# Kernel tuning notes

Measured on AMD Instinct MI355X. Metric: run time of the kernel, lower is better.

The kernel has to match this reference:

```python
import jax, jax.numpy as jnp
import numpy as np

NUM_HEADS = 8
ROPE_BASE = 10000.0


def _rope(x):
    # x: [B, S, E]; standard interleaved rotary embedding applied on full embed dim
    B, S, E = x.shape
    half = E // 2
    inv_freq = 1.0 / (ROPE_BASE ** (jnp.arange(0, half, dtype=jnp.float32) * 2.0 / E))
    freqs = jnp.arange(S, dtype=jnp.float32)[:, None] * inv_freq[None, :]  # [S, E/2]
    cos = jnp.cos(freqs)[None]  # [1, S, E/2]
    sin = jnp.sin(freqs)[None]
    x1 = x[..., 0::2]
    x2 = x[..., 1::2]
    r1 = x1 * cos - x2 * sin
    r2 = x1 * sin + x2 * cos
    return jnp.stack([r1, r2], axis=-1).reshape(B, S, E)


def setup_inputs() -> dict:
    key = jax.random.key(0)
    ks = jax.random.split(key, 7)
    B, S, E = 2, 4096, 512
    q = jax.random.normal(ks[0], (B, S, E), dtype=jnp.float32)
    k = jax.random.normal(ks[1], (B, S, E), dtype=jnp.float32)
    v = jax.random.normal(ks[2], (B, S, E), dtype=jnp.float32)
    scale = 1.0 / np.sqrt(E)
    in_proj_w = jax.random.normal(ks[3], (3 * E, E), dtype=jnp.float32) * scale
    in_proj_b = jnp.zeros((3 * E,), dtype=jnp.float32)
    out_proj_w = jax.random.normal(ks[4], (E, E), dtype=jnp.float32) * scale
    out_proj_b = jnp.zeros((E,), dtype=jnp.float32)
    return {"query": q, "key": k, "value": v,
            "in_proj_w": in_proj_w, "in_proj_b": in_proj_b,
            "out_proj_w": out_proj_w, "out_proj_b": out_proj_b}


def reference(query, key, value, in_proj_w, in_proj_b, out_proj_w, out_proj_b):
    B, S, E = query.shape
    H = NUM_HEADS
    D = E // H
    # RoPE applied before projection, as in the original module
    q_in = _rope(query)
    k_in = _rope(key)
    Wq, Wk, Wv = jnp.split(in_proj_w, 3, axis=0)
    bq, bk, bv = jnp.split(in_proj_b, 3, axis=0)
    q = (q_in @ Wq.T + bq).reshape(B, S, H, D).transpose(0, 2, 1, 3)  # [B,H,S,D]
    k = (k_in @ Wk.T + bk).reshape(B, S, H, D).transpose(0, 2, 1, 3)
    v = (value @ Wv.T + bv).reshape(B, S, H, D).transpose(0, 2, 1, 3)
    scores = jnp.einsum('bhqd,bhkd->bhqk', q, k) / jnp.sqrt(jnp.asarray(D, q.dtype))
    weights = jax.nn.softmax(scores, axis=-1)  # [B,H,S,S]
    ctx = jnp.einsum('bhqk,bhkd->bhqd', weights, v)  # [B,H,S,D]
    ctx = ctx.transpose(0, 2, 1, 3).reshape(B, S, E)
    attn_output = ctx @ out_proj_w.T + out_proj_b
    attn_weights = weights.mean(axis=1)  # averaged over heads (need_weights=True default)
    return attn_output, attn_weights
```

## Files before the change

kernel.cpp:

```cpp
#include <hip/hip_runtime.h>
#include <stdint.h>
#include <stddef.h>


#define B_ 2
#define S_ 4096
#define E_ 512
#define H_ 8
#define D_ 64
#define BS_ (B_*S_)

typedef __attribute__((ext_vector_type(8)))  short short8;
typedef __attribute__((ext_vector_type(4)))  float f32x4;
typedef __attribute__((ext_vector_type(16))) float f32x16;
typedef __attribute__((ext_vector_type(4)))  int   i32x4;

#define DEVFN static __device__ __forceinline__

DEVFN short f2bf(float x) {
    unsigned u = __builtin_bit_cast(unsigned, x);
    u += 0x7fffu + ((u >> 16) & 1u);
    return (short)(u >> 16);
}

__global__ void k_cstable(float2* __restrict__ cs) {
    int pos = blockIdx.x;
    int i   = threadIdx.x;
    double ang = (double)pos * exp(-0.035977892078031968 * (double)i);
    cs[pos * 256 + i] = make_float2((float)cos(ang), (float)sin(ang));
}

__global__ void k_rope2(const float* __restrict__ q, const float* __restrict__ k,
                        const float2* __restrict__ cs,
                        short* __restrict__ Aq, short* __restrict__ Ak) {
    int row = blockIdx.x;
    int i   = threadIdx.x;
    const float* x   = blockIdx.y ? k  : q;
    short*       out = blockIdx.y ? Ak : Aq;
    int s = row & (S_ - 1);
    float2 c = cs[s * 256 + i];
    float x1 = x[(size_t)row * E_ + 2 * i];
    float x2 = x[(size_t)row * E_ + 2 * i + 1];
    float r1 = x1 * c.x - x2 * c.y;
    float r2 = x1 * c.y + x2 * c.x;
    unsigned pk = ((unsigned)(unsigned short)f2bf(r1)) |
                  (((unsigned)(unsigned short)f2bf(r2)) << 16);
    *reinterpret_cast<unsigned*>(out + (size_t)row * E_ + 2 * i) = pk;
}

#define NV8  (BS_ * E_ / 8)
#define NW18 (3 * E_ * E_ / 8)
#define NW28 (E_ * E_ / 8)
__global__ void k_cast3(const float* __restrict__ v, const float* __restrict__ in_w,
                        const float* __restrict__ out_w,
                        short* __restrict__ Av, short* __restrict__ Wall,
                        short* __restrict__ Wo) {
    int i = blockIdx.x * 256 + threadIdx.x;
    const float* src; short* dst; int j;
    if (i < NV8)               { src = v;     dst = Av;   j = i; }
    else if (i < NV8 + NW18)   { src = in_w;  dst = Wall; j = i - NV8; }
    else if (i < NV8 + NW18 + NW28) { src = out_w; dst = Wo; j = i - NV8 - NW18; }
    else return;
    f32x4 a = *reinterpret_cast<const f32x4*>(src + (size_t)j * 8);
    f32x4 b = *reinterpret_cast<const f32x4*>(src + (size_t)j * 8 + 4);
    short8 o;
#pragma unroll
    for (int t = 0; t < 4; t++) { o[t] = f2bf(a[t]); o[4 + t] = f2bf(b[t]); }
    *reinterpret_cast<short8*>(dst + (size_t)j * 8) = o;
}

__global__ __launch_bounds__(256) void k_gemm_qkv(
    const short* __restrict__ Aq, const short* __restrict__ Ak,
    const short* __restrict__ Av, const short* __restrict__ Wall,
    const float* __restrict__ in_b,
    short* __restrict__ Qh, short* __restrict__ Kh, short* __restrict__ vtmp) {
    __shared__ short sA[128 * 72];
    __shared__ short sB[128 * 72];
    int z = blockIdx.z;
    const short* A  = (z == 0) ? Aq : (z == 1) ? Ak : Av;
    const short* Bw = Wall + (size_t)z * E_ * E_;
    const float* bias = in_b + z * E_;
    int tid = threadIdx.x;
    int lane = tid & 63, wv = tid >> 6;
    int lane16 = lane & 15, lgrp = lane >> 4;
    int row0 = blockIdx.y * 128;
    int col0 = blockIdx.x * 128;
    int wr = (wv >> 1) * 64, wc = (wv & 1) * 64;

    f32x4 acc[4][4];
#pragma unroll
    for (int i = 0; i < 4; i++)
#pragma unroll
        for (int j = 0; j < 4; j++)
#pragma unroll
            for (int r = 0; r < 4; r++) acc[i][j][r] = 0.f;

    for (int kt = 0; kt < 8; ++kt) {
        short8 va[4], vb[4];
#pragma unroll
        for (int i = 0; i < 4; i++) {
            int ch = i * 256 + tid;
            int r = ch >> 3, ce = (ch & 7) * 8;
            va[i] = *reinterpret_cast<const short8*>(A  + (size_t)(row0 + r) * E_ + kt * 64 + ce);
            vb[i] = *reinterpret_cast<const short8*>(Bw + (size_t)(col0 + r) * E_ + kt * 64 + ce);
        }
        __syncthreads();
#pragma unroll
        for (int i = 0; i < 4; i++) {
            int ch = i * 256 + tid;
            int r = ch >> 3, ce = (ch & 7) * 8;
            *reinterpret_cast<short8*>(sA + r * 72 + ce) = va[i];
            *reinterpret_cast<short8*>(sB + r * 72 + ce) = vb[i];
        }
        __syncthreads();
#pragma unroll
        for (int ks = 0; ks < 2; ++ks) {
            short8 af[4];
#pragma unroll
            for (int i = 0; i < 4; i++)
                af[i] = *reinterpret_cast<const short8*>(sA + (wr + i * 16 + lane16) * 72 + ks * 32 + lgrp * 8);
#pragma unroll
            for (int j = 0; j < 4; j++) {
                short8 bf = *reinterpret_cast<const short8*>(sB + (wc + j * 16 + lane16) * 72 + ks * 32 + lgrp * 8);
#pragma unroll
                for (int i = 0; i < 4; i++)
                    acc[i][j] = __builtin_amdgcn_mfma_f32_16x16x32_bf16(af[i], bf, acc[i][j], 0, 0, 0);
            }
        }
    }
#pragma unroll
    for (int i = 0; i < 4; i++) {
#pragma unroll
        for (int j = 0; j < 4; j++) {
            int col = col0 + wc + j * 16 + lane16;
            float bv = bias[col];
#pragma unroll
            for (int r = 0; r < 4; r++) {
                int row = row0 + wr + i * 16 + lgrp * 4 + r;
                float vx = acc[i][j][r] + bv;
                if (z == 0) {
                    vx *= 0.18033688011112042f;
                    int b = row >> 12, s = row & (S_ - 1);
                    int h = col >> 6, d = col & 63;
                    Qh[((size_t)(b * H_ + h) * S_ + s) * D_ + d] = f2bf(vx);
                } else if (z == 1) {
                    int b = row >> 12, s = row & (S_ - 1);
                    int h = col >> 6, d = col & 63;
                    Kh[((size_t)(b * H_ + h) * S_ + s) * D_ + d] = f2bf(vx);
                } else {
                    vtmp[(size_t)row * E_ + col] = f2bf(vx);
                }
            }
        }
    }
}

__global__ __launch_bounds__(256) void k_gemm_out(
    const short* __restrict__ A, const short* __restrict__ Bw,
    const float* __restrict__ bias, float* __restrict__ out_f) {
    __shared__ short sA[128 * 72];
    __shared__ short sB[128 * 72];
    int tid = threadIdx.x;
    int lane = tid & 63, wv = tid >> 6;
    int lane16 = lane & 15, lgrp = lane >> 4;
    int row0 = blockIdx.y * 128;
    int col0 = blockIdx.x * 128;
    int wr = (wv >> 1) * 64, wc = (wv & 1) * 64;

    f32x4 acc[4][4];
#pragma unroll
    for (int i = 0; i < 4; i++)
#pragma unroll
        for (int j = 0; j < 4; j++)
#pragma unroll
            for (int r = 0; r < 4; r++) acc[i][j][r] = 0.f;

    for (int kt = 0; kt < 8; ++kt) {
        short8 va[4], vb[4];
#pragma unroll
        for (int i = 0; i < 4; i++) {
            int ch = i * 256 + tid;
            int r = ch >> 3, ce = (ch & 7) * 8;
            va[i] = *reinterpret_cast<const short8*>(A  + (size_t)(row0 + r) * E_ + kt * 64 + ce);
            vb[i] = *reinterpret_cast<const short8*>(Bw + (size_t)(col0 + r) * E_ + kt * 64 + ce);
        }
        __syncthreads();
#pragma unroll
        for (int i = 0; i < 4; i++) {
            int ch = i * 256 + tid;
            int r = ch >> 3, ce = (ch & 7) * 8;
            *reinterpret_cast<short8*>(sA + r * 72 + ce) = va[i];
            *reinterpret_cast<short8*>(sB + r * 72 + ce) = vb[i];
        }
        __syncthreads();
#pragma unroll
        for (int ks = 0; ks < 2; ++ks) {
            short8 af[4];
#pragma unroll
            for (int i = 0; i < 4; i++)
                af[i] = *reinterpret_cast<const short8*>(sA + (wr + i * 16 + lane16) * 72 + ks * 32 + lgrp * 8);
#pragma unroll
            for (int j = 0; j < 4; j++) {
                short8 bf = *reinterpret_cast<const short8*>(sB + (wc + j * 16 + lane16) * 72 + ks * 32 + lgrp * 8);
#pragma unroll
                for (int i = 0; i < 4; i++)
                    acc[i][j] = __builtin_amdgcn_mfma_f32_16x16x32_bf16(af[i], bf, acc[i][j], 0, 0, 0);
            }
        }
    }
#pragma unroll
    for (int i = 0; i < 4; i++) {
#pragma unroll
        for (int j = 0; j < 4; j++) {
            int col = col0 + wc + j * 16 + lane16;
            float bv = bias[col];
#pragma unroll
            for (int r = 0; r < 4; r++) {
                int row = row0 + wr + i * 16 + lgrp * 4 + r;
                out_f[(size_t)row * E_ + col] = acc[i][j][r] + bv;
            }
        }
    }
}

__global__ void k_transpose_v(const short* __restrict__ vin, short* __restrict__ Vt) {
    __shared__ short t[64][66];
    int bid = blockIdx.x;
    int st = bid & 63, h = (bid >> 6) & 7, b = bid >> 9;
    int tid = threadIdx.x;
#pragma unroll
    for (int i = 0; i < 16; i++) {
        int idx = i * 256 + tid;
        int sl = idx >> 6, d = idx & 63;
        t[sl][d] = vin[((size_t)(b * S_ + st * 64 + sl)) * E_ + h * 64 + d];
    }
    __syncthreads();
#pragma unroll
    for (int i = 0; i < 16; i++) {
        int idx = i * 256 + tid;
        int dl = idx >> 6, sl = idx & 63;
        Vt[((size_t)(b * H_ + h) * 64 + dl) * S_ + st * 64 + sl] = t[sl][dl];
    }
}

DEVFN short8 lds_rd(const short* buf, int row, int colb) {
    return *reinterpret_cast<const short8*>(
        (const char*)buf + row * 128 + (colb ^ ((row & 7) << 4)));
}

__global__ __launch_bounds__(256) void k_flash(
    const short* __restrict__ Qh, const short* __restrict__ Kh,
    const short* __restrict__ Vt, short* __restrict__ ctxb,
    float* __restrict__ Lrow) {
    __shared__ short kbuf[2][64 * 64];
    __shared__ short vbuf[2][64 * 64];
    __shared__ short ob[4][32 * 72];
    int tid = threadIdx.x, lane = tid & 63, wv = tid >> 6;
    int l31 = lane & 31, hi = lane >> 5;
    int gid = blockIdx.x;
    int qt = gid & 31, h = (gid >> 5) & 7, b = gid >> 8;
    int bh = b * H_ + h;
    int qrow0 = qt * 128 + wv * 32;
    const short* Qp = Qh + ((size_t)bh * S_ + qrow0) * D_;
    const short* Kp = Kh + (size_t)bh * S_ * D_;
    const short* Vp = Vt + (size_t)bh * 64 * S_;

    short8 qf[4];
#pragma unroll
    for (int ds = 0; ds < 4; ds++)
        qf[ds] = *reinterpret_cast<const short8*>(
            Qp + (size_t)l31 * D_ + ds * 16 + hi * 8);

    f32x16 ctx0, ctx1;
#pragma unroll
    for (int r = 0; r < 16; r++) { ctx0[r] = 0.f; ctx1[r] = 0.f; }
    float lsum = 0.f;

    int srow = wv * 16 + (lane >> 3);
    int scol = (lane & 7) * 8;
    int swz  = (scol * 2) ^ ((lane >> 3) << 4);

    short8 kst[2], vst[2];
#define STAGE_LOAD(kb_) do {                                                     \
    int nb_ = (kb_);                                                             \
    _Pragma("unroll") for (int ci = 0; ci < 2; ci++) {                           \
        int r_ = srow + ci * 8;                                                  \
        kst[ci] = *reinterpret_cast<const short8*>(Kp + (size_t)(nb_ + r_) * D_ + scol); \
        vst[ci] = *reinterpret_cast<const short8*>(Vp + (size_t)r_ * S_ + nb_ + scol);   \
    } } while (0)
#define STAGE_WRITE(d_) do {                                                     \
    _Pragma("unroll") for (int ci = 0; ci < 2; ci++) {                           \
        int r_ = srow + ci * 8;                                                  \
        *reinterpret_cast<short8*>((char*)kbuf[d_] + r_ * 128 + swz) = kst[ci];  \
        *reinterpret_cast<short8*>((char*)vbuf[d_] + r_ * 128 + swz) = vst[ci];  \
    } } while (0)

    STAGE_LOAD(0);
    STAGE_WRITE(0);
    __syncthreads();
    int cur = 0;

    for (int kt = 0; kt < 64; ++kt) {
        if (kt < 63) STAGE_LOAD((kt + 1) * 64);

        f32x16 s0, s1;
#pragma unroll
        for (int r = 0; r < 16; r++) { s0[r] = 0.f; s1[r] = 0.f; }
#pragma unroll
        for (int ds = 0; ds < 4; ds++) {
            short8 k0 = lds_rd(kbuf[cur], l31,      ds * 32 + hi * 16);
            short8 k1 = lds_rd(kbuf[cur], 32 + l31, ds * 32 + hi * 16);
            s0 = __builtin_amdgcn_mfma_f32_32x32x16_bf16(k0, qf[ds], s0, 0, 0, 0);
            s1 = __builtin_amdgcn_mfma_f32_32x32x16_bf16(k1, qf[ds], s1, 0, 0, 0);
        }
#pragma unroll
        for (int r = 0; r < 16; r++) { s0[r] = __builtin_amdgcn_exp2f(s0[r]); lsum += s0[r]; }
#pragma unroll
        for (int r = 0; r < 16; r++) { s1[r] = __builtin_amdgcn_exp2f(s1[r]); lsum += s1[r]; }

        int w[16];
#pragma unroll
        for (int t = 0; t < 8; t++) {
            asm("v_cvt_pk_bf16_f32 %0, %1, %2" : "=v"(w[t])     : "v"(s0[2 * t]), "v"(s0[2 * t + 1]));
            asm("v_cvt_pk_bf16_f32 %0, %1, %2" : "=v"(w[8 + t]) : "v"(s1[2 * t]), "v"(s1[2 * t + 1]));
        }
        short8 pf[4];
#pragma unroll
        for (int g = 0; g < 4; g++) {
            int a0 = w[g * 4 + 0], b0 = w[g * 4 + 2];
            int a1 = w[g * 4 + 1], b1 = w[g * 4 + 3];
            asm("v_permlane32_swap_b32 %0, %1" : "+v"(a0), "+v"(b0));
            asm("v_permlane32_swap_b32 %0, %1" : "+v"(a1), "+v"(b1));
            i32x4 t4 = {a0, a1, b0, b1};
            pf[g] = __builtin_bit_cast(short8, t4);
        }
#pragma unroll
        for (int ks = 0; ks < 4; ks++) {
            short8 v0 = lds_rd(vbuf[cur], l31,      ks * 32 + hi * 16);
            short8 v1 = lds_rd(vbuf[cur], 32 + l31, ks * 32 + hi * 16);
            ctx0 = __builtin_amdgcn_mfma_f32_32x32x16_bf16(v0, pf[ks], ctx0, 0, 0, 0);
            ctx1 = __builtin_amdgcn_mfma_f32_32x32x16_bf16(v1, pf[ks], ctx1, 0, 0, 0);
        }
        if (kt < 63) STAGE_WRITE(cur ^ 1);
        __syncthreads();
        cur ^= 1;
    }

    float l_run = lsum + __shfl_xor(lsum, 32);
    float invl = 1.0f / l_run;
    short* obw = &ob[wv][0];
#pragma unroll
    for (int n = 0; n < 2; n++) {
#pragma unroll
        for (int t = 0; t < 8; t++) {
            float a  = (n ? ctx1[2 * t]     : ctx0[2 * t])     * invl;
            float bb = (n ? ctx1[2 * t + 1] : ctx0[2 * t + 1]) * invl;
            int wd;
            asm("v_cvt_pk_bf16_f32 %0, %1, %2" : "=v"(wd) : "v"(a), "v"(bb));
            int d = n * 32 + ((2 * t) & 3) + 8 * ((2 * t) >> 2) + 4 * hi;
            *reinterpret_cast<int*>(obw + l31 * 72 + d) = wd;
        }
    }
    __syncthreads();
    {
        int q = lane >> 1, half = lane & 1;
        size_t gbase = ((size_t)b * S_ + qrow0 + q) * E_ + h * 64 + half * 32;
#pragma unroll
        for (int j = 0; j < 4; j++) {
            short8 vvv = *reinterpret_cast<const short8*>(obw + q * 72 + half * 32 + j * 8);
            *reinterpret_cast<short8*>(ctxb + gbase + j * 8) = vvv;
        }
    }
    if (lane < 32)
        Lrow[(size_t)bh * S_ + qrow0 + lane] = l_run;
#undef STAGE_LOAD
#undef STAGE_WRITE
}

__global__ __launch_bounds__(256) void k_weights(
    const short* __restrict__ Qh, const short* __restrict__ Kh,
    const float* __restrict__ Lrow,
    float* __restrict__ outw) {
    __shared__ short Kt[2][64 * 64];
    __shared__ short Qt[2][128 * 64];
    __shared__ float c_lds[1024];
    int tid = threadIdx.x, lane = tid & 63, wv = tid >> 6;
    int l31 = lane & 31, hi = lane >> 5;
    int gid = blockIdx.x;
    int kc = gid & 63, qt = (gid >> 6) & 31, b = gid >> 11;
    int k0 = kc * 64;
    int qblk = qt * 128;
    int qrow0 = qblk + wv * 32;

    {
        int e0 = tid * 4;
        int hh = e0 >> 7, qq = e0 & 127;
        size_t base = ((size_t)(b * H_ + hh)) * S_ + qblk + qq;
        f32x4 lv = *reinterpret_cast<const f32x4*>(&Lrow[base]);
        f32x4 cc;
#pragma unroll
        for (int j = 0; j < 4; j++) cc[j] = -3.0f - __log2f(lv[j]);
        *reinterpret_cast<f32x4*>(&c_lds[e0]) = cc;
    }

    int srow8 = lane >> 3;
    int scol  = (lane & 7) * 8;
    int swz   = (scol * 2) ^ (srow8 << 4);

    const short* Kbase = Kh + ((size_t)(b * H_) * S_ + k0) * D_;
    const short* Qbase = Qh + ((size_t)(b * H_) * S_ + qblk) * D_;

    short8 kst[2], qst[4];
#pragma unroll
    for (int ci = 0; ci < 2; ci++)
        kst[ci] = *reinterpret_cast<const short8*>(
            Kbase + (size_t)(wv * 16 + ci * 8 + srow8) * D_ + scol);
#pragma unroll
    for (int ci = 0; ci < 4; ci++)
        qst[ci] = *reinterpret_cast<const short8*>(
            Qbase + (size_t)(wv * 32 + ci * 8 + srow8) * D_ + scol);
#pragma unroll
    for (int ci = 0; ci < 2; ci++)
        *reinterpret_cast<short8*>((char*)Kt[0] + (wv * 16 + ci * 8 + srow8) * 128 + swz) = kst[ci];
#pragma unroll
    for (int ci = 0; ci < 4; ci++)
        *reinterpret_cast<short8*>((char*)Qt[0] + (wv * 32 + ci * 8 + srow8) * 128 + swz) = qst[ci];
    __syncthreads();

    f32x16 w0, w1;
#pragma unroll
    for (int r = 0; r < 16; r++) { w0[r] = 0.f; w1[r] = 0.f; }

    int cur = 0;
    for (int h = 0; h < H_; ++h) {
        if (h < 7) {
            const short* kp = Kbase + (size_t)(h + 1) * S_ * D_;
            const short* qp = Qbase + (size_t)(h + 1) * S_ * D_;
#pragma unroll
            for (int ci = 0; ci < 2; ci++)
                kst[ci] = *reinterpret_cast<const short8*>(
                    kp + (size_t)(wv * 16 + ci * 8 + srow8) * D_ + scol);
#pragma unroll
            for (int ci = 0; ci < 4; ci++)
                qst[ci] = *reinterpret_cast<const short8*>(
                    qp + (size_t)(wv * 32 + ci * 8 + srow8) * D_ + scol);
        }
        f32x16 s0, s1;
#pragma unroll
        for (int g = 0; g < 4; g++) {
            f32x4 ci4 = *reinterpret_cast<const f32x4*>(
                &c_lds[h * 128 + wv * 32 + 4 * hi + 8 * g]);
#pragma unroll
            for (int j = 0; j < 4; j++) { s0[g * 4 + j] = ci4[j]; s1[g * 4 + j] = ci4[j]; }
        }
#pragma unroll
        for (int ks = 0; ks < 4; ks++) {
            short8 aq = lds_rd(Qt[cur], wv * 32 + l31, ks * 32 + hi * 16);
            short8 b0 = lds_rd(Kt[cur], l31,           ks * 32 + hi * 16);
            short8 b1 = lds_rd(Kt[cur], 32 + l31,      ks * 32 + hi * 16);
            s0 = __builtin_amdgcn_mfma_f32_32x32x16_bf16(aq, b0, s0, 0, 0, 0);
            s1 = __builtin_amdgcn_mfma_f32_32x32x16_bf16(aq, b1, s1, 0, 0, 0);
        }
#pragma unroll
        for (int r = 0; r < 16; r++) {
            w0[r] += __builtin_amdgcn_exp2f(s0[r]);
            w1[r] += __builtin_amdgcn_exp2f(s1[r]);
        }
        if (h < 7) {
#pragma unroll
            for (int ci = 0; ci < 2; ci++)
                *reinterpret_cast<short8*>((char*)Kt[cur ^ 1] + (wv * 16 + ci * 8 + srow8) * 128 + swz) = kst[ci];
#pragma unroll
            for (int ci = 0; ci < 4; ci++)
                *reinterpret_cast<short8*>((char*)Qt[cur ^ 1] + (wv * 32 + ci * 8 + srow8) * 128 + swz) = qst[ci];
        }
        __syncthreads();
        cur ^= 1;
    }
#pragma unroll
    for (int r = 0; r < 16; r++) {
        int qrow = qrow0 + (r & 3) + 8 * (r >> 2) + 4 * hi;
        float* op = outw + ((size_t)b * S_ + qrow) * (size_t)S_ + k0;
        op[l31]      = w0[r];
        op[32 + l31] = w1[r];
    }
}

extern "C" void kernel_launch(void* const* d_in, const int* in_sizes, int n_in,
                              void* d_out, int out_size, void* d_ws, size_t ws_size,
                              hipStream_t stream) {
    (void)in_sizes; (void)n_in; (void)out_size; (void)ws_size;
    const float* q     = (const float*)d_in[0];
    const float* k     = (const float*)d_in[1];
    const float* v     = (const float*)d_in[2];
    const float* in_w  = (const float*)d_in[3];
    const float* in_b  = (const float*)d_in[4];
    const float* out_w = (const float*)d_in[5];
    const float* out_b = (const float*)d_in[6];
    float* out  = (float*)d_out;
    float* outw = out + (size_t)B_ * S_ * E_;

    char* ws = (char*)d_ws;
    size_t off = 0;
    auto alloc = [&](size_t bytes) { void* p = ws + off; off += (bytes + 255) & ~(size_t)255; return p; };

    float2* cs   = (float2*)alloc((size_t)S_ * 256 * 8);
    short*  Aq   = (short*) alloc((size_t)BS_ * E_ * 2);
    short*  Ak   = (short*) alloc((size_t)BS_ * E_ * 2);
    short*  Av   = (short*) alloc((size_t)BS_ * E_ * 2);
    short*  Wall = (short*) alloc((size_t)3 * E_ * E_ * 2);
    short*  Wo   = (short*) alloc((size_t)E_ * E_ * 2);
    short*  Qh   = (short*) alloc((size_t)B_ * H_ * S_ * D_ * 2);
    short*  Kh   = (short*) alloc((size_t)B_ * H_ * S_ * D_ * 2);
    short*  vtmp = (short*) alloc((size_t)BS_ * E_ * 2);
    short*  Vt   = (short*) alloc((size_t)B_ * H_ * D_ * S_ * 2);
    short*  ctxb = (short*) alloc((size_t)BS_ * E_ * 2);
    float*  Lrow = (float*) alloc((size_t)B_ * H_ * S_ * 4);

    k_cstable<<<S_, 256, 0, stream>>>(cs);
    k_rope2<<<dim3(BS_, 2), 256, 0, stream>>>(q, k, cs, Aq, Ak);
    k_cast3<<<(NV8 + NW18 + NW28 + 255) / 256, 256, 0, stream>>>(v, in_w, out_w, Av, Wall, Wo);

    k_gemm_qkv<<<dim3(E_ / 128, BS_ / 128, 3), 256, 0, stream>>>(
        Aq, Ak, Av, Wall, in_b, Qh, Kh, vtmp);
    k_transpose_v<<<B_ * H_ * (S_ / 64), 256, 0, stream>>>(vtmp, Vt);
    k_flash<<<B_ * H_ * (S_ / 128), 256, 0, stream>>>(Qh, Kh, Vt, ctxb, Lrow);
    k_gemm_out<<<dim3(E_ / 128, BS_ / 128), 256, 0, stream>>>(ctxb, Wo, out_b, out);
    k_weights<<<B_ * (S_ / 128) * (S_ / 64), 256, 0, stream>>>(Qh, Kh, Lrow, outw);
}
```

Baseline: 239.8 us.

## Fuse V transpose into QKV GEMM epilogue and prioritize MFMA phases in flash

The V projection GEMM now transposes its output tile through shared memory and writes directly into the head-major Vt layout. This removes the separate transpose kernel, its launch and the round trip through the intermediate buffer. Separately, the flash attention loop raises wave priority around the two MFMA sections with s_setprio, intended to favour matrix-core issue over other waves. The extra shared-memory transpose and barriers add some cost to the GEMM epilogue.

```diff
diff --git a/kernel.cpp b/kernel.cpp
--- a/kernel.cpp
+++ b/kernel.cpp
@@ -73,9 +73,10 @@
     const short* __restrict__ Aq, const short* __restrict__ Ak,
     const short* __restrict__ Av, const short* __restrict__ Wall,
     const float* __restrict__ in_b,
-    short* __restrict__ Qh, short* __restrict__ Kh, short* __restrict__ vtmp) {
-    __shared__ short sA[128 * 72];
-    __shared__ short sB[128 * 72];
+    short* __restrict__ Qh, short* __restrict__ Kh, short* __restrict__ Vt) {
+    __shared__ short smem2[2][128 * 72];
+    short* sA = smem2[0];
+    short* sB = smem2[1];
     int z = blockIdx.z;
     const short* A  = (z == 0) ? Aq : (z == 1) ? Ak : Av;
     const short* Bw = Wall + (size_t)z * E_ * E_;
@@ -128,6 +129,37 @@
             }
         }
     }
+    if (z == 2) {
+        __syncthreads();
+        short* tr = &smem2[0][0];
+#pragma unroll
+        for (int i = 0; i < 4; i++) {
+#pragma unroll
+            for (int j = 0; j < 4; j++) {
+                int cl = wc + j * 16 + lane16;
+                float bv = bias[col0 + cl];
+#pragma unroll
+                for (int r = 0; r < 4; r++) {
+                    int rl = wr + i * 16 + lgrp * 4 + r;
+                    tr[cl * 144 + rl] = f2bf(acc[i][j][r] + bv);
+                }
+            }
+        }
+        __syncthreads();
+        {
+            int el = tid >> 1, shalf = (tid & 1) * 64;
+            int colg = col0 + el;
+            int h = colg >> 6, d = colg & 63;
+            int b = row0 >> 12, s0 = row0 & (S_ - 1);
+            size_t dst = ((size_t)(b * H_ + h) * D_ + d) * S_ + s0 + shalf;
+#pragma unroll
+            for (int jj = 0; jj < 8; jj++) {
+                short8 vv = *reinterpret_cast<const short8*>(tr + el * 144 + shalf + jj * 8);
+                *reinterpret_cast<short8*>(Vt + dst + jj * 8) = vv;
+            }
+        }
+        return;
+    }
 #pragma unroll
     for (int i = 0; i < 4; i++) {
 #pragma unroll
@@ -138,17 +170,13 @@
             for (int r = 0; r < 4; r++) {
                 int row = row0 + wr + i * 16 + lgrp * 4 + r;
                 float vx = acc[i][j][r] + bv;
+                int b = row >> 12, s = row & (S_ - 1);
+                int h = col >> 6, d = col & 63;
                 if (z == 0) {
                     vx *= 0.18033688011112042f;
-                    int b = row >> 12, s = row & (S_ - 1);
-                    int h = col >> 6, d = col & 63;
                     Qh[((size_t)(b * H_ + h) * S_ + s) * D_ + d] = f2bf(vx);
-                } else if (z == 1) {
-                    int b = row >> 12, s = row & (S_ - 1);
-                    int h = col >> 6, d = col & 63;
+                } else {
                     Kh[((size_t)(b * H_ + h) * S_ + s) * D_ + d] = f2bf(vx);
-                } else {
-                    vtmp[(size_t)row * E_ + col] = f2bf(vx);
                 }
             }
         }
@@ -220,26 +248,6 @@
                 out_f[(size_t)row * E_ + col] = acc[i][j][r] + bv;
             }
         }
-    }
-}
-
-__global__ void k_transpose_v(const short* __restrict__ vin, short* __restrict__ Vt) {
-    __shared__ short t[64][66];
-    int bid = blockIdx.x;
-    int st = bid & 63, h = (bid >> 6) & 7, b = bid >> 9;
-    int tid = threadIdx.x;
-#pragma unroll
-    for (int i = 0; i < 16; i++) {
-        int idx = i * 256 + tid;
-        int sl = idx >> 6, d = idx & 63;
-        t[sl][d] = vin[((size_t)(b * S_ + st * 64 + sl)) * E_ + h * 64 + d];
-    }
-    __syncthreads();
-#pragma unroll
-    for (int i = 0; i < 16; i++) {
-        int idx = i * 256 + tid;
-        int dl = idx >> 6, sl = idx & 63;
-        Vt[((size_t)(b * H_ + h) * 64 + dl) * S_ + st * 64 + sl] = t[sl][dl];
     }
 }
 
@@ -306,6 +314,7 @@
         f32x16 s0, s1;
 #pragma unroll
         for (int r = 0; r < 16; r++) { s0[r] = 0.f; s1[r] = 0.f; }
+        __builtin_amdgcn_s_setprio(1);
 #pragma unroll
         for (int ds = 0; ds < 4; ds++) {
             short8 k0 = lds_rd(kbuf[cur], l31,      ds * 32 + hi * 16);
@@ -313,6 +322,7 @@
             s0 = __builtin_amdgcn_mfma_f32_32x32x16_bf16(k0, qf[ds], s0, 0, 0, 0);
             s1 = __builtin_amdgcn_mfma_f32_32x32x16_bf16(k1, qf[ds], s1, 0, 0, 0);
         }
+        __builtin_amdgcn_s_setprio(0);
 #pragma unroll
         for (int r = 0; r < 16; r++) { s0[r] = __builtin_amdgcn_exp2f(s0[r]); lsum += s0[r]; }
 #pragma unroll
@@ -334,6 +344,7 @@
             i32x4 t4 = {a0, a1, b0, b1};
             pf[g] = __builtin_bit_cast(short8, t4);
         }
+        __builtin_amdgcn_s_setprio(1);
 #pragma unroll
         for (int ks = 0; ks < 4; ks++) {
             short8 v0 = lds_rd(vbuf[cur], l31,      ks * 32 + hi * 16);
@@ -341,6 +352,7 @@
             ctx0 = __builtin_amdgcn_mfma_f32_32x32x16_bf16(v0, pf[ks], ctx0, 0, 0, 0);
             ctx1 = __builtin_amdgcn_mfma_f32_32x32x16_bf16(v1, pf[ks], ctx1, 0, 0, 0);
         }
+        __builtin_amdgcn_s_setprio(0);
         if (kt < 63) STAGE_WRITE(cur ^ 1);
         __syncthreads();
         cur ^= 1;
@@ -512,7 +524,6 @@
     short*  Wo   = (short*) alloc((size_t)E_ * E_ * 2);
     short*  Qh   = (short*) alloc((size_t)B_ * H_ * S_ * D_ * 2);
     short*  Kh   = (short*) alloc((size_t)B_ * H_ * S_ * D_ * 2);
-    short*  vtmp = (short*) alloc((size_t)BS_ * E_ * 2);
     short*  Vt   = (short*) alloc((size_t)B_ * H_ * D_ * S_ * 2);
     short*  ctxb = (short*) alloc((size_t)BS_ * E_ * 2);
     float*  Lrow = (float*) alloc((size_t)B_ * H_ * S_ * 4);
@@ -522,8 +533,7 @@
     k_cast3<<<(NV8 + NW18 + NW28 + 255) / 256, 256, 0, stream>>>(v, in_w, out_w, Av, Wall, Wo);
 
     k_gemm_qkv<<<dim3(E_ / 128, BS_ / 128, 3), 256, 0, stream>>>(
-        Aq, Ak, Av, Wall, in_b, Qh, Kh, vtmp);
-    k_transpose_v<<<B_ * H_ * (S_ / 64), 256, 0, stream>>>(vtmp, Vt);
+        Aq, Ak, Av, Wall, in_b, Qh, Kh, Vt);
     k_flash<<<B_ * H_ * (S_ / 128), 256, 0, stream>>>(Qh, Kh, Vt, ctxb, Lrow);
     k_gemm_out<<<dim3(E_ / 128, BS_ / 128), 256, 0, stream>>>(ctxb, Wo, out_b, out);
     k_weights<<<B_ * (S_ / 128) * (S_ / 64), 256, 0, stream>>>(Qh, Kh, Lrow, outw);
```

Result: no change. 240.9 us (+0.5%).
